# Performance work log

Measured on AMD Instinct MI355X. Metric: run time of the kernel, lower is better.

## Reference

```python
import jax, jax.numpy as jnp
import numpy as np

H = 128

def _gine_conv(x, ei, ea, w1, b1, w2, b2):
    # GINEConv (eps=0): out = MLP(x + sum_{j->i} relu(x_j + e_ji))
    src, dst = ei[0], ei[1]
    m = jax.nn.relu(x[src] + ea)                      # [E, H]
    agg = jax.ops.segment_sum(m, dst, num_segments=x.shape[0])
    h = x + agg
    return jax.nn.relu(h @ w1 + b1) @ w2 + b2

def _bn(x, gamma, beta, eps=1e-5):
    # BatchNorm1d over node dim, batch statistics (training mode)
    mu = jnp.mean(x, axis=0)
    var = jnp.mean((x - mu) ** 2, axis=0)
    return gamma * (x - mu) * jax.lax.rsqrt(var + eps) + beta

def _scatter_mean(vals, ids, mask, n):
    w = mask.astype(vals.dtype)
    s = jax.ops.segment_sum(vals * w[:, None], ids, num_segments=n)
    c = jax.ops.segment_sum(w, ids, num_segments=n)
    return s / jnp.maximum(c, 1.0)[:, None]


def setup_inputs() -> dict:
    key = jax.random.key(0)
    ks = jax.random.split(key, 20)
    Nf, Nt, S, K = 320000, 100000, 20000, 16
    Ei, Eg = 1280000, 800000
    sc = 1.0 / np.sqrt(H)
    inp = {}
    inp["h_flat"] = jax.random.normal(ks[0], (Nf, H), jnp.float32)
    inp["intra_ei"] = jax.random.randint(ks[1], (2, Ei), 0, Nf, jnp.int32)
    inp["ea_flat"] = jax.random.normal(ks[2], (Ei, H), jnp.float32)
    inp["valid"] = jnp.ones((Nf,), jnp.bool_)
    inp["node_ids"] = jax.random.randint(ks[3], (Nf,), 0, Nt, jnp.int32)
    inp["N_total"] = Nt
    inp["edge_index"] = jax.random.randint(ks[4], (2, Eg), 0, Nt, jnp.int32)
    inp["edge_attr"] = jax.random.normal(ks[5], (Eg, H), jnp.float32)
    inp["sub_batch"] = jax.random.randint(ks[6], (Nf,), 0, S, jnp.int32)
    inp["S"] = S
    inp["k"] = K
    inp["root_flat_idx"] = jax.random.randint(ks[7], (S,), 0, Nf, jnp.int32)
    inp["is_root"] = jnp.zeros((Nf,), jnp.bool_)
    # parameters
    inp["local_w1"] = jax.random.normal(ks[8], (H, H), jnp.float32) * sc
    inp["local_b1"] = jnp.zeros((H,), jnp.float32)
    inp["local_w2"] = jax.random.normal(ks[9], (H, H), jnp.float32) * sc
    inp["local_b2"] = jnp.zeros((H,), jnp.float32)
    inp["local_gamma"] = jnp.ones((H,), jnp.float32)
    inp["local_beta"] = jnp.zeros((H,), jnp.float32)
    inp["global_w1"] = jax.random.normal(ks[10], (H, H), jnp.float32) * sc
    inp["global_b1"] = jnp.zeros((H,), jnp.float32)
    inp["global_w2"] = jax.random.normal(ks[11], (H, H), jnp.float32) * sc
    inp["global_b2"] = jnp.zeros((H,), jnp.float32)
    inp["global_gamma"] = jnp.ones((H,), jnp.float32)
    inp["global_beta"] = jnp.zeros((H,), jnp.float32)
    inp["skip_w"] = jax.random.normal(ks[12], (H, H), jnp.float32) * sc
    inp["skip_b"] = jnp.zeros((H,), jnp.float32)
    inp["vv_w"] = jax.random.normal(ks[13], (H, H), jnp.float32) * sc
    inp["vv_b"] = jnp.zeros((H,), jnp.float32)
    inp["kk_w"] = jax.random.normal(ks[14], (H, H), jnp.float32) * sc
    inp["kk_b"] = jnp.zeros((H,), jnp.float32)
    return inp


def reference(h_flat, intra_ei, ea_flat, valid, node_ids, N_total, edge_index, edge_attr,
              sub_batch, S, k, root_flat_idx, is_root,
              local_w1, local_b1, local_w2, local_b2, local_gamma, local_beta,
              global_w1, global_b1, global_w2, global_b2, global_gamma, global_beta,
              skip_w, skip_b, vv_w, vv_b, kk_w, kk_b):
    valid_f = valid.astype(h_flat.dtype)[:, None]
    clamped_ids = jnp.maximum(node_ids, 0)
    valid_mask = node_ids >= 0

    h_skip = (h_flat @ skip_w + skip_b) * valid_f

    h1 = _gine_conv(h_flat, intra_ei, ea_flat, local_w1, local_b1, local_w2, local_b2)
    h1 = _bn(h1, local_gamma, local_beta) * valid_f

    x_sum = _scatter_mean(h_flat, clamped_ids, valid_mask, N_total)   # [N_total, H]
    h2 = _gine_conv(x_sum, edge_index, edge_attr, global_w1, global_b1, global_w2, global_b2)
    h2 = _bn(h2, global_gamma, global_beta)[clamped_ids] * valid_f

    root_ids = node_ids[root_flat_idx]
    root_valid = root_ids >= 0
    x_vv_canonical = _scatter_mean(h_flat[root_flat_idx], jnp.maximum(root_ids, 0), root_valid, N_total)
    x_vv = (x_vv_canonical[clamped_ids] @ vv_w + vv_b) * valid_f

    x_kk = (h_flat[root_flat_idx[sub_batch]] @ kk_w + kk_b) * valid_f

    out = jax.nn.relu(h_skip + h1 + h2 + x_vv + x_kk)
    # dropout p=0.0 -> identity
    return out * valid_f
```

## Files before the change

kernel.cpp:

```cpp
#include <hip/hip_runtime.h>

#define H    128
#define HQ   32
#define TM   64
#define NT   100000
#define XS   136


typedef __attribute__((ext_vector_type(8))) short short8;
typedef __attribute__((ext_vector_type(4))) float f32x4;

static __host__ int cdiv(long a, long b) { return (int)((a + b - 1) / b); }
static __host__ char* alignp(char* p) {
    return (char*)(((uintptr_t)p + 255) & ~(uintptr_t)255);
}

__device__ inline unsigned short f2bf(float f) {
    unsigned u = __float_as_uint(f);
    unsigned r = u + 0x7FFFu + ((u >> 16) & 1u);
    return (unsigned short)(r >> 16);
}
__device__ inline float bf2f(unsigned short u) {
    return __uint_as_float((unsigned)u << 16);
}

__global__ __launch_bounds__(256) void k_cvt(
    const float* __restrict__ in, unsigned short* __restrict__ out, long n8)
{
    long i = (long)blockIdx.x * 256 + threadIdx.x;
    if (i >= n8) return;
    float4 a = ((const float4*)in)[2 * i];
    float4 b = ((const float4*)in)[2 * i + 1];
    ushort4 lo; lo.x = f2bf(a.x); lo.y = f2bf(a.y); lo.z = f2bf(a.z); lo.w = f2bf(a.w);
    ushort4 hi; hi.x = f2bf(b.x); hi.y = f2bf(b.y); hi.z = f2bf(b.z); hi.w = f2bf(b.w);
    ((ushort4*)out)[2 * i]     = lo;
    ((ushort4*)out)[2 * i + 1] = hi;
}

struct WJobs { const float* src[7]; };

__global__ __launch_bounds__(256) void k_cvtw(WJobs wj, unsigned short* __restrict__ dstBase)
{
    int w = blockIdx.x >> 4, chunk = blockIdx.x & 15;
    int i = chunk * 256 + threadIdx.x;
    int k = i >> 5, n4 = (i & 31) * 4;
    float4 v = ((const float4*)wj.src[w])[i];
    unsigned short* dst = dstBase + (size_t)w * H * H;
    dst[(n4 + 0) * H + k] = f2bf(v.x);
    dst[(n4 + 1) * H + k] = f2bf(v.y);
    dst[(n4 + 2) * H + k] = f2bf(v.z);
    dst[(n4 + 3) * H + k] = f2bf(v.w);
}

struct CsrJobs {
    const int* ids[4];
    const int* rfi;
    int* cnt[4];
    int* rp[4];
    int* cur[4];
    int* eid[4];
    int  E[4];
    int  N[4];
    int  histBase[5];
    int  scanBase[5];
};

__device__ inline int csr_id(const CsrJobs& jb, int sg, int e)
{
    if (sg == 3) {
        int nid = jb.ids[2][jb.rfi[e]];
        return nid > 0 ? nid : 0;
    }
    return jb.ids[sg][e];
}

__global__ __launch_bounds__(256) void k_hist4(CsrJobs jb)
{
    int b = blockIdx.x, sg = 0;
    while (b >= jb.histBase[sg + 1]) ++sg;
    int e = (b - jb.histBase[sg]) * 256 + threadIdx.x;
    if (e < jb.E[sg]) atomicAdd(&jb.cnt[sg][csr_id(jb, sg, e)], 1);
}

__global__ __launch_bounds__(256) void k_scanA4(CsrJobs jb, int* __restrict__ parts)
{
    int b = blockIdx.x, sg = 0;
    while (b >= jb.scanBase[sg + 1]) ++sg;
    int lb = b - jb.scanBase[sg];
    const int* cnt = jb.cnt[sg];
    int* rowptr = jb.rp[sg];
    int N = jb.N[sg];
    int* partials = parts + sg * 256;

    __shared__ int lsum[256];
    int tid = threadIdx.x;
    int base = lb * 2048 + tid * 8;
    int v[8];
    int tsum = 0;
#pragma unroll
    for (int i = 0; i < 8; ++i) {
        int idx = base + i;
        int t = (idx < N) ? cnt[idx] : 0;
        v[i] = tsum;
        tsum += t;
    }
    lsum[tid] = tsum;
    __syncthreads();
    for (int off = 1; off < 256; off <<= 1) {
        int t = (tid >= off) ? lsum[tid - off] : 0;
        __syncthreads();
        lsum[tid] += t;
        __syncthreads();
    }
    int texcl = lsum[tid] - tsum;
#pragma unroll
    for (int i = 0; i < 8; ++i) {
        int idx = base + i;
        if (idx < N) rowptr[idx] = v[i] + texcl;
    }
    if (tid == 255) partials[lb] = lsum[255];
}

__global__ __launch_bounds__(256) void k_scanB4(CsrJobs jb, int* __restrict__ parts)
{
    int sg = blockIdx.x;
    int P = jb.scanBase[sg + 1] - jb.scanBase[sg];
    int* partials = parts + sg * 256;
    int* rowptr = jb.rp[sg];
    int N = jb.N[sg];

    __shared__ int lsum[256];
    int tid = threadIdx.x;
    int val = (tid < P) ? partials[tid] : 0;
    lsum[tid] = val;
    __syncthreads();
    for (int off = 1; off < 256; off <<= 1) {
        int t = (tid >= off) ? lsum[tid - off] : 0;
        __syncthreads();
        lsum[tid] += t;
        __syncthreads();
    }
    if (tid < P) partials[tid] = lsum[tid] - val;
    if (tid == 255) rowptr[N] = lsum[255];
}

__global__ __launch_bounds__(256) void k_scanC4(CsrJobs jb, const int* __restrict__ parts)
{
    int b = blockIdx.x, sg = 0;
    while (b >= jb.scanBase[sg + 1]) ++sg;
    int lb = b - jb.scanBase[sg];
    int off = parts[sg * 256 + lb];
    int N = jb.N[sg];
    int* rowptr = jb.rp[sg];
    int* cursor = jb.cur[sg];
    int base = lb * 2048;
    for (int i = threadIdx.x; i < 2048; i += 256) {
        int g = base + i;
        if (g < N) {
            int v = rowptr[g] + off;
            rowptr[g] = v;
            cursor[g] = v;
        }
    }
}

__global__ __launch_bounds__(256) void k_fillperm4(CsrJobs jb)
{
    int b = blockIdx.x, sg = 0;
    while (b >= jb.histBase[sg + 1]) ++sg;
    int e = (b - jb.histBase[sg]) * 256 + threadIdx.x;
    if (e < jb.E[sg]) {
        int pos = atomicAdd(&jb.cur[sg][csr_id(jb, sg, e)], 1);
        jb.eid[sg][pos] = e;
    }
}

__global__ __launch_bounds__(256) void k_csr_edge_agg(
    const unsigned short* __restrict__ X, const float* __restrict__ EA,
    const int* __restrict__ src, const int* __restrict__ eid,
    const int* __restrict__ rowptr, unsigned short* __restrict__ OUT, int N)
{
    int idx = blockIdx.x * 256 + threadIdx.x;
    int n = idx >> 5, l = idx & 31;
    if (n >= N) return;
    int beg = rowptr[n], end = rowptr[n + 1];
    float4 acc = {0.f, 0.f, 0.f, 0.f};
    for (int c0 = beg; c0 < end; c0 += 32) {
        int cnt = min(32, end - c0);
        int e_l = 0, s_l = 0;
        if (l < cnt) { e_l = eid[c0 + l]; s_l = src[e_l]; }
        for (int j = 0; j < cnt; ++j) {
            int e = __shfl(e_l, j, 32);
            int s = __shfl(s_l, j, 32);
            float4 a = ((const float4*)(EA + (size_t)e * H))[l];
            ushort4 h = ((const ushort4*)(X + (size_t)s * H))[l];
            acc.x += fmaxf(bf2f(h.x) + a.x, 0.f);
            acc.y += fmaxf(bf2f(h.y) + a.y, 0.f);
            acc.z += fmaxf(bf2f(h.z) + a.z, 0.f);
            acc.w += fmaxf(bf2f(h.w) + a.w, 0.f);
        }
    }
    ushort4 o;
    o.x = f2bf(acc.x); o.y = f2bf(acc.y); o.z = f2bf(acc.z); o.w = f2bf(acc.w);
    ((ushort4*)(OUT + (size_t)n * H))[l] = o;
}

__global__ __launch_bounds__(256) void k_csr_mean(
    const unsigned short* __restrict__ X, const int* __restrict__ eid,
    const int* __restrict__ rowptr, unsigned short* __restrict__ OUT, int N)
{
    int idx = blockIdx.x * 256 + threadIdx.x;
    int n = idx >> 5, l = idx & 31;
    if (n >= N) return;
    int beg = rowptr[n], end = rowptr[n + 1];
    float4 acc = {0.f, 0.f, 0.f, 0.f};
    for (int c0 = beg; c0 < end; c0 += 32) {
        int cnt = min(32, end - c0);
        int f_l = 0;
        if (l < cnt) f_l = eid[c0 + l];
        for (int j = 0; j < cnt; ++j) {
            int fi = __shfl(f_l, j, 32);
            ushort4 h = ((const ushort4*)(X + (size_t)fi * H))[l];
            acc.x += bf2f(h.x); acc.y += bf2f(h.y);
            acc.z += bf2f(h.z); acc.w += bf2f(h.w);
        }
    }
    float inv = 1.0f / fmaxf((float)(end - beg), 1.0f);
    ushort4 o;
    o.x = f2bf(acc.x * inv); o.y = f2bf(acc.y * inv);
    o.z = f2bf(acc.z * inv); o.w = f2bf(acc.w * inv);
    ((ushort4*)(OUT + (size_t)n * H))[l] = o;
}

__device__ inline void stage_x_copy(
    unsigned short* sX, const unsigned short* X1, const int* gidx,
    int r0, int M, int tid)
{
    int r = tid >> 2, q = tid & 3;
    int row = r0 + r;
    unsigned short* dst = &sX[r * XS + q * 32];
    if (row < M) {
        int sr = gidx ? gidx[row] : row;
        const ushort4* xp = (const ushort4*)(X1 + (size_t)sr * H + q * 32);
#pragma unroll
        for (int i = 0; i < 8; ++i) *(ushort4*)(dst + i * 4) = xp[i];
    } else {
#pragma unroll
        for (int i = 0; i < 8; ++i) *(ushort4*)(dst + i * 4) = ushort4{0, 0, 0, 0};
    }
}

__device__ inline void stage_x_sum(
    unsigned short* sX, const unsigned short* X1, const unsigned short* X2,
    int r0, int M, int tid)
{
    int r = tid >> 2, q = tid & 3;
    int row = r0 + r;
    unsigned short* dst = &sX[r * XS + q * 32];
    if (row < M) {
        const ushort4* xp = (const ushort4*)(X1 + (size_t)row * H + q * 32);
        const ushort4* yp = (const ushort4*)(X2 + (size_t)row * H + q * 32);
#pragma unroll
        for (int i = 0; i < 8; ++i) {
            ushort4 a = xp[i], b = yp[i];
            ushort4 o;
            o.x = f2bf(bf2f(a.x) + bf2f(b.x));
            o.y = f2bf(bf2f(a.y) + bf2f(b.y));
            o.z = f2bf(bf2f(a.z) + bf2f(b.z));
            o.w = f2bf(bf2f(a.w) + bf2f(b.w));
            *(ushort4*)(dst + i * 4) = o;
        }
    } else {
#pragma unroll
        for (int i = 0; i < 8; ++i) *(ushort4*)(dst + i * 4) = ushort4{0, 0, 0, 0};
    }
}

__device__ inline void stage_wt_pre(
    unsigned short* sWT, const unsigned short* WT, int tid)
{
    for (int i = tid; i < H * HQ; i += 256) {
        int n = i >> 5, kq = i & 31;
        *(ushort4*)&sWT[n * XS + kq * 4] = ((const ushort4*)WT)[i];
    }
}

__global__ __launch_bounds__(256) void k_gemm(
    const unsigned short* __restrict__ X1, const int* __restrict__ gidx,
    const unsigned short* __restrict__ WT, const float* __restrict__ B,
    unsigned short* __restrict__ OUT, int M)
{
    __shared__ unsigned short sX[TM * XS];
    __shared__ unsigned short sWT[H * XS];
    __shared__ float sB[H];
    int tid = threadIdx.x;
    int r0 = blockIdx.x * TM;

    stage_x_copy(sX, X1, gidx, r0, M, tid);
    stage_wt_pre(sWT, WT, tid);
    if (tid < 32) ((float4*)sB)[tid] = ((const float4*)B)[tid];
    __syncthreads();

    int wv = tid >> 6, l = tid & 63;
    int lr = l & 15, hi = l >> 4, lk = hi * 8;

    f32x4 acc[8];
#pragma unroll
    for (int ct = 0; ct < 8; ++ct) acc[ct] = {0.f, 0.f, 0.f, 0.f};
#pragma unroll
    for (int kk = 0; kk < 4; ++kk) {
        short8 a = *(const short8*)&sX[(wv * 16 + lr) * XS + kk * 32 + lk];
#pragma unroll
        for (int ct = 0; ct < 8; ++ct) {
            short8 b = *(const short8*)&sWT[(ct * 16 + lr) * XS + kk * 32 + lk];
            acc[ct] = __builtin_amdgcn_mfma_f32_16x16x32_bf16(a, b, acc[ct], 0, 0, 0);
        }
    }

    int orow0 = r0 + wv * 16 + hi * 4;
#pragma unroll
    for (int ct = 0; ct < 8; ++ct) {
        int col = ct * 16 + lr;
        float bias = sB[col];
#pragma unroll
        for (int j = 0; j < 4; ++j) {
            int row = orow0 + j;
            if (row >= M) continue;
            OUT[(size_t)row * H + col] = f2bf(acc[ct][j] + bias);
        }
    }
}

__global__ __launch_bounds__(256) void k_mean_gemm(
    const unsigned short* __restrict__ X, const int* __restrict__ eid,
    const int* __restrict__ rowmap, const int* __restrict__ rowptr,
    const unsigned short* __restrict__ WT, const float* __restrict__ B,
    unsigned short* __restrict__ OUT, int M)
{
    __shared__ unsigned short sX[TM * XS];
    __shared__ unsigned short sWT[H * XS];
    __shared__ float sB[H];
    int tid = threadIdx.x;
    int r0 = blockIdx.x * TM;

    {
        int r = tid >> 2, q = tid & 3;
        int row = r0 + r;
        float4 m[8];
#pragma unroll
        for (int i = 0; i < 8; ++i) m[i] = {0.f, 0.f, 0.f, 0.f};
        int cnt = 0;
        if (row < M) {
            int beg = rowptr[row], end = rowptr[row + 1];
            cnt = end - beg;
            for (int j = beg; j < end; ++j) {
                int fi = rowmap[eid[j]];
                const ushort4* hp = (const ushort4*)(X + (size_t)fi * H + q * 32);
#pragma unroll
                for (int i = 0; i < 8; ++i) {
                    ushort4 v = hp[i];
                    m[i].x += bf2f(v.x); m[i].y += bf2f(v.y);
                    m[i].z += bf2f(v.z); m[i].w += bf2f(v.w);
                }
            }
        }
        float inv = 1.0f / fmaxf((float)cnt, 1.0f);
        unsigned short* dst = &sX[r * XS + q * 32];
#pragma unroll
        for (int i = 0; i < 8; ++i) {
            ushort4 b;
            b.x = f2bf(m[i].x * inv); b.y = f2bf(m[i].y * inv);
            b.z = f2bf(m[i].z * inv); b.w = f2bf(m[i].w * inv);
            *(ushort4*)(dst + i * 4) = b;
        }
    }
    stage_wt_pre(sWT, WT, tid);
    if (tid < 32) ((float4*)sB)[tid] = ((const float4*)B)[tid];
    __syncthreads();

    int wv = tid >> 6, l = tid & 63;
    int lr = l & 15, hi = l >> 4, lk = hi * 8;

    f32x4 acc[8];
#pragma unroll
    for (int ct = 0; ct < 8; ++ct) acc[ct] = {0.f, 0.f, 0.f, 0.f};
#pragma unroll
    for (int kk = 0; kk < 4; ++kk) {
        short8 a = *(const short8*)&sX[(wv * 16 + lr) * XS + kk * 32 + lk];
#pragma unroll
        for (int ct = 0; ct < 8; ++ct) {
            short8 b = *(const short8*)&sWT[(ct * 16 + lr) * XS + kk * 32 + lk];
            acc[ct] = __builtin_amdgcn_mfma_f32_16x16x32_bf16(a, b, acc[ct], 0, 0, 0);
        }
    }

    int orow0 = r0 + wv * 16 + hi * 4;
#pragma unroll
    for (int ct = 0; ct < 8; ++ct) {
        int col = ct * 16 + lr;
        float bias = sB[col];
#pragma unroll
        for (int j = 0; j < 4; ++j) {
            int row = orow0 + j;
            if (row >= M) continue;
            OUT[(size_t)row * H + col] = f2bf(acc[ct][j] + bias);
        }
    }
}

__global__ __launch_bounds__(256) void k_mlp(
    const unsigned short* __restrict__ X1, const unsigned short* __restrict__ X2,
    const unsigned short* __restrict__ W1T, const float* __restrict__ B1,
    const unsigned short* __restrict__ W2T, const float* __restrict__ B2,
    unsigned short* __restrict__ OUT, int M,
    float* __restrict__ gs, float* __restrict__ gs2)
{
    __shared__ unsigned short sX[TM * XS];
    __shared__ unsigned short sWT[H * XS];
    __shared__ float sB1[H], sB2[H];
    __shared__ float sS[H], sS2[H];
    int tid = threadIdx.x;
    int r0 = blockIdx.x * TM;

    stage_x_sum(sX, X1, X2, r0, M, tid);
    stage_wt_pre(sWT, W1T, tid);
    if (tid < 32) ((float4*)sB1)[tid] = ((const float4*)B1)[tid];
    else if (tid < 64) ((float4*)sB2)[tid - 32] = ((const float4*)B2)[tid - 32];
    if (tid >= 64 && tid < 192) { sS[tid - 64] = 0.f; sS2[tid - 64] = 0.f; }
    __syncthreads();

    int wv = tid >> 6, l = tid & 63;
    int lr = l & 15, hi = l >> 4, lk = hi * 8;
    int rloc = wv * 16 + hi * 4;

    f32x4 acc[8];
#pragma unroll
    for (int ct = 0; ct < 8; ++ct) acc[ct] = {0.f, 0.f, 0.f, 0.f};
#pragma unroll
    for (int kk = 0; kk < 4; ++kk) {
        short8 a = *(const short8*)&sX[(wv * 16 + lr) * XS + kk * 32 + lk];
#pragma unroll
        for (int ct = 0; ct < 8; ++ct) {
            short8 b = *(const short8*)&sWT[(ct * 16 + lr) * XS + kk * 32 + lk];
            acc[ct] = __builtin_amdgcn_mfma_f32_16x16x32_bf16(a, b, acc[ct], 0, 0, 0);
        }
    }
    __syncthreads();

#pragma unroll
    for (int ct = 0; ct < 8; ++ct) {
        int c = ct * 16 + lr;
        float b1v = sB1[c];
#pragma unroll
        for (int j = 0; j < 4; ++j) {
            float v = fmaxf(acc[ct][j] + b1v, 0.f);
            int mybf = (int)f2bf(v);
            int other = __shfl_xor(mybf, 1);
            if (!(lr & 1)) {
                unsigned packed = (unsigned)(unsigned short)mybf
                                | ((unsigned)(unsigned short)other << 16);
                *(unsigned*)&sX[(rloc + j) * XS + c] = packed;
            }
        }
        acc[ct] = {0.f, 0.f, 0.f, 0.f};
    }
    stage_wt_pre(sWT, W2T, tid);
    __syncthreads();

#pragma unroll
    for (int kk = 0; kk < 4; ++kk) {
        short8 a = *(const short8*)&sX[(wv * 16 + lr) * XS + kk * 32 + lk];
#pragma unroll
        for (int ct = 0; ct < 8; ++ct) {
            short8 b = *(const short8*)&sWT[(ct * 16 + lr) * XS + kk * 32 + lk];
            acc[ct] = __builtin_amdgcn_mfma_f32_16x16x32_bf16(a, b, acc[ct], 0, 0, 0);
        }
    }

    int orow0 = r0 + rloc;
#pragma unroll
    for (int ct = 0; ct < 8; ++ct) {
        int col = ct * 16 + lr;
        float b2v = sB2[col];
        float ps = 0.f, ps2 = 0.f;
#pragma unroll
        for (int j = 0; j < 4; ++j) {
            int row = orow0 + j;
            if (row >= M) continue;
            float o = acc[ct][j] + b2v;
            OUT[(size_t)row * H + col] = f2bf(o);
            ps += o; ps2 += o * o;
        }
        atomicAdd(&sS[col], ps);
        atomicAdd(&sS2[col], ps2);
    }
    __syncthreads();
    if (tid < H) {
        unsafeAtomicAdd(&gs[tid], sS[tid]);
        unsafeAtomicAdd(&gs2[tid], sS2[tid]);
    }
}

__global__ __launch_bounds__(256) void k_final_gemm(
    const unsigned short* __restrict__ Hf,
    const unsigned short* __restrict__ SKWT, const float* __restrict__ SKB,
    const unsigned short* __restrict__ h1raw, const unsigned short* __restrict__ h2raw,
    const unsigned short* __restrict__ vvy, const unsigned short* __restrict__ kky,
    const int* __restrict__ node_ids, const int* __restrict__ sub_batch,
    const float* __restrict__ stats,
    const float* __restrict__ lg, const float* __restrict__ lbe,
    const float* __restrict__ gg, const float* __restrict__ gbe,
    float n1, float n2,
    float* __restrict__ OUT, int M)
{
    __shared__ unsigned short sX[TM * XS];
    __shared__ unsigned short sWT[H * XS];
    __shared__ float sP[5 * H];
    int tid = threadIdx.x;
    int r0 = blockIdx.x * TM;

    stage_x_copy(sX, Hf, nullptr, r0, M, tid);
    stage_wt_pre(sWT, SKWT, tid);
    if (tid < H) {
        float mu = stats[tid] / n1;
        float var = stats[H + tid] / n1 - mu * mu;
        float sc = lg[tid] * rsqrtf(var + 1e-5f);
        sP[tid] = sc; sP[H + tid] = lbe[tid] - mu * sc;
        mu = stats[2 * H + tid] / n2;
        var = stats[3 * H + tid] / n2 - mu * mu;
        sc = gg[tid] * rsqrtf(var + 1e-5f);
        sP[2 * H + tid] = sc; sP[3 * H + tid] = gbe[tid] - mu * sc;
    } else if (tid < H + 32) {
        ((float4*)(sP + 4 * H))[tid - H] = ((const float4*)SKB)[tid - H];
    }
    __syncthreads();

    int wv = tid >> 6, l = tid & 63;
    int lr = l & 15, hi = l >> 4, lk = hi * 8;

    f32x4 acc[8];
#pragma unroll
    for (int ct = 0; ct < 8; ++ct) acc[ct] = {0.f, 0.f, 0.f, 0.f};
#pragma unroll
    for (int kk = 0; kk < 4; ++kk) {
        short8 a = *(const short8*)&sX[(wv * 16 + lr) * XS + kk * 32 + lk];
#pragma unroll
        for (int ct = 0; ct < 8; ++ct) {
            short8 b = *(const short8*)&sWT[(ct * 16 + lr) * XS + kk * 32 + lk];
            acc[ct] = __builtin_amdgcn_mfma_f32_16x16x32_bf16(a, b, acc[ct], 0, 0, 0);
        }
    }
    __syncthreads();

    float* sF = (float*)sWT;
    int rloc0 = wv * 16 + hi * 4;
#pragma unroll
    for (int ct = 0; ct < 8; ++ct) {
        int col = ct * 16 + lr;
        float skbv = sP[4 * H + col];
#pragma unroll
        for (int j = 0; j < 4; ++j)
            sF[(rloc0 + j) * 130 + col] = acc[ct][j] + skbv;
    }
    __syncthreads();

    {
        int r = tid >> 2, q = tid & 3;
        int row = r0 + r;
        if (row < M) {
            int nid = node_ids[row];
            size_t cid = (size_t)(nid > 0 ? nid : 0);
            size_t sb  = (size_t)sub_batch[row];
            const ushort4* h1p = (const ushort4*)(h1raw + (size_t)row * H + q * 32);
            const ushort4* h2p = (const ushort4*)(h2raw + cid * H + q * 32);
            const ushort4* vvp = (const ushort4*)(vvy + cid * H + q * 32);
            const ushort4* kkp = (const ushort4*)(kky + sb * H + q * 32);
            float* op = OUT + (size_t)row * H + q * 32;
            const float* fr = &sF[r * 130 + q * 32];
#pragma unroll
            for (int i = 0; i < 8; ++i) {
                ushort4 a = h1p[i], b = h2p[i], c = vvp[i], d = kkp[i];
                int cb = q * 32 + i * 4;
                float4 o;
                o.x = fr[i * 4 + 0] + bf2f(a.x) * sP[cb + 0] + sP[H + cb + 0]
                    + bf2f(b.x) * sP[2 * H + cb + 0] + sP[3 * H + cb + 0]
                    + bf2f(c.x) + bf2f(d.x);
                o.y = fr[i * 4 + 1] + bf2f(a.y) * sP[cb + 1] + sP[H + cb + 1]
                    + bf2f(b.y) * sP[2 * H + cb + 1] + sP[3 * H + cb + 1]
                    + bf2f(c.y) + bf2f(d.y);
                o.z = fr[i * 4 + 2] + bf2f(a.z) * sP[cb + 2] + sP[H + cb + 2]
                    + bf2f(b.z) * sP[2 * H + cb + 2] + sP[3 * H + cb + 2]
                    + bf2f(c.z) + bf2f(d.z);
                o.w = fr[i * 4 + 3] + bf2f(a.w) * sP[cb + 3] + sP[H + cb + 3]
                    + bf2f(b.w) * sP[2 * H + cb + 3] + sP[3 * H + cb + 3]
                    + bf2f(c.w) + bf2f(d.w);
                o.x = fmaxf(o.x, 0.f); o.y = fmaxf(o.y, 0.f);
                o.z = fmaxf(o.z, 0.f); o.w = fmaxf(o.w, 0.f);
                ((float4*)op)[i] = o;
            }
        }
    }
}

extern "C" void kernel_launch(void* const* d_in, const int* in_sizes, int n_in,
                              void* d_out, int out_size, void* d_ws, size_t ws_size,
                              hipStream_t stream)
{
    const float* h_flat        = (const float*)d_in[0];
    const int*   intra_ei      = (const int*)d_in[1];
    const float* ea_flat       = (const float*)d_in[2];
    const int*   node_ids      = (const int*)d_in[4];
    const int*   edge_index    = (const int*)d_in[6];
    const float* edge_attr     = (const float*)d_in[7];
    const int*   sub_batch     = (const int*)d_in[8];
    const int*   root_flat_idx = (const int*)d_in[11];
    const float* lw1 = (const float*)d_in[13];
    const float* lb1 = (const float*)d_in[14];
    const float* lw2 = (const float*)d_in[15];
    const float* lb2 = (const float*)d_in[16];
    const float* lg  = (const float*)d_in[17];
    const float* lbe = (const float*)d_in[18];
    const float* gw1 = (const float*)d_in[19];
    const float* gb1 = (const float*)d_in[20];
    const float* gw2 = (const float*)d_in[21];
    const float* gb2 = (const float*)d_in[22];
    const float* gg  = (const float*)d_in[23];
    const float* gbe = (const float*)d_in[24];
    const float* skw = (const float*)d_in[25];
    const float* skb = (const float*)d_in[26];
    const float* vvw = (const float*)d_in[27];
    const float* vvb = (const float*)d_in[28];
    const float* kkw = (const float*)d_in[29];
    const float* kkb = (const float*)d_in[30];

    const int Nf = in_sizes[0] / H;
    const int Ei = in_sizes[2] / H;
    const int Eg = in_sizes[7] / H;
    const int S  = in_sizes[11];

    char* w = (char*)d_ws;
    unsigned short* hbf  = (unsigned short*)w; w += (size_t)Nf * H * 2;
    unsigned short* buf1 = (unsigned short*)w; w += (size_t)Nf * H * 2;
    unsigned short* xsum = (unsigned short*)w; w += (size_t)NT * H * 2;
    unsigned short* buf2 = (unsigned short*)w; w += (size_t)NT * H * 2;
    unsigned short* vvy  = (unsigned short*)w; w += (size_t)NT * H * 2;
    unsigned short* kbuf = (unsigned short*)w; w += (size_t)S * H * 2;
    unsigned short* wtb  = (unsigned short*)w; w += (size_t)7 * H * H * 2;
    w = alignp(w);
    int* cntAll = (int*)w; w += ((size_t)Nf + 3 * (size_t)NT) * 4;
    float* stats = (float*)w; w += 4 * H * 4;
    w = alignp(w);
    int* rpA  = (int*)w; w += ((size_t)Nf + 1) * 4;  w = alignp(w);
    int* rpB  = (int*)w; w += ((size_t)NT + 1) * 4;  w = alignp(w);
    int* rpC  = (int*)w; w += ((size_t)NT + 1) * 4;  w = alignp(w);
    int* rpD  = (int*)w; w += ((size_t)NT + 1) * 4;  w = alignp(w);
    int* curA = (int*)w; w += (size_t)Nf * 4;
    int* curB = (int*)w; w += (size_t)NT * 4;
    int* curC = (int*)w; w += (size_t)NT * 4;
    int* curD = (int*)w; w += (size_t)NT * 4;
    int* eidA = (int*)w; w += (size_t)Ei * 4;
    int* eidB = (int*)w; w += (size_t)Eg * 4;
    int* eidC = (int*)w; w += (size_t)Nf * 4;
    int* eidD = (int*)w; w += (size_t)S * 4;
    int* parts = (int*)w; w += 4 * 256 * 4;
    int* cntA = cntAll;
    int* cntB = cntA + Nf;
    int* cntC = cntB + NT;
    int* cntD = cntC + NT;

    hipMemsetAsync(cntAll, 0, ((size_t)Nf + 3 * (size_t)NT) * 4 + 4 * H * 4, stream);

    k_cvt<<<cdiv((long)Nf * H / 8, 256), 256, 0, stream>>>(
        h_flat, hbf, (long)Nf * H / 8);
    WJobs wj;
    wj.src[0] = lw1; wj.src[1] = lw2; wj.src[2] = gw1; wj.src[3] = gw2;
    wj.src[4] = skw; wj.src[5] = vvw; wj.src[6] = kkw;
    k_cvtw<<<7 * 16, 256, 0, stream>>>(wj, wtb);

    CsrJobs jb;
    jb.ids[0] = intra_ei + Ei;  jb.ids[1] = edge_index + Eg;
    jb.ids[2] = node_ids;       jb.ids[3] = nullptr;
    jb.rfi = root_flat_idx;
    jb.cnt[0] = cntA; jb.cnt[1] = cntB; jb.cnt[2] = cntC; jb.cnt[3] = cntD;
    jb.rp[0]  = rpA;  jb.rp[1]  = rpB;  jb.rp[2]  = rpC;  jb.rp[3]  = rpD;
    jb.cur[0] = curA; jb.cur[1] = curB; jb.cur[2] = curC; jb.cur[3] = curD;
    jb.eid[0] = eidA; jb.eid[1] = eidB; jb.eid[2] = eidC; jb.eid[3] = eidD;
    jb.E[0] = Ei; jb.E[1] = Eg; jb.E[2] = Nf; jb.E[3] = S;
    jb.N[0] = Nf; jb.N[1] = NT; jb.N[2] = NT; jb.N[3] = NT;
    jb.histBase[0] = 0;
    for (int i = 0; i < 4; ++i) jb.histBase[i + 1] = jb.histBase[i] + cdiv(jb.E[i], 256);
    jb.scanBase[0] = 0;
    for (int i = 0; i < 4; ++i) jb.scanBase[i + 1] = jb.scanBase[i] + cdiv(jb.N[i], 2048);

    k_hist4<<<jb.histBase[4], 256, 0, stream>>>(jb);
    k_scanA4<<<jb.scanBase[4], 256, 0, stream>>>(jb, parts);
    k_scanB4<<<4, 256, 0, stream>>>(jb, parts);
    k_scanC4<<<jb.scanBase[4], 256, 0, stream>>>(jb, parts);
    k_fillperm4<<<jb.histBase[4], 256, 0, stream>>>(jb);

    k_csr_mean<<<cdiv((long)NT * 32, 256), 256, 0, stream>>>(
        hbf, eidC, rpC, xsum, NT);
    k_csr_edge_agg<<<cdiv((long)Nf * 32, 256), 256, 0, stream>>>(
        hbf, ea_flat, intra_ei, eidA, rpA, buf1, Nf);
    k_csr_edge_agg<<<cdiv((long)NT * 32, 256), 256, 0, stream>>>(
        xsum, edge_attr, edge_index, eidB, rpB, buf2, NT);

    k_mlp<<<cdiv(Nf, TM), 256, 0, stream>>>(hbf, buf1, wtb + 0 * H * H, lb1,
                                            wtb + 1 * H * H, lb2,
                                            buf1, Nf, stats, stats + H);
    k_mlp<<<cdiv(NT, TM), 256, 0, stream>>>(xsum, buf2, wtb + 2 * H * H, gb1,
                                            wtb + 3 * H * H, gb2,
                                            buf2, NT, stats + 2 * H, stats + 3 * H);

    k_mean_gemm<<<cdiv(NT, TM), 256, 0, stream>>>(
        hbf, eidD, root_flat_idx, rpD, wtb + 5 * H * H, vvb, vvy, NT);
    k_gemm<<<cdiv(S, TM), 256, 0, stream>>>(hbf, root_flat_idx,
                                            wtb + 6 * H * H, kkb, kbuf, S);

    k_final_gemm<<<cdiv(Nf, TM), 256, 0, stream>>>(
        hbf, wtb + 4 * H * H, skb, buf1, buf2, vvy, kbuf, node_ids, sub_batch,
        stats, lg, lbe, gg, gbe, (float)Nf, (float)NT, (float*)d_out, Nf);
}
```

Baseline: 1.295 ms.

## Fuse GINE edge aggregation into MLP staging and merge conversion kernels

Removes the separate CSR edge-aggregation kernels and does the gather/relu/sum inside the MLP kernel's shared-memory staging, so the aggregated bf16 buffer is never written to or read back from global memory. Each thread now handles a quarter row and walks all incoming edges serially. This replaces the old layout where 32 lanes split a row and shared index loads via shuffles, so per-thread latency and load imbalance go up. It also merges the activation and weight bf16 conversion kernels into one launch. Rounding changes slightly: x + agg is now summed in fp32 before a single bf16 rounding.

```diff
diff --git a/kernel.cpp b/kernel.cpp
--- a/kernel.cpp
+++ b/kernel.cpp
@@ -24,32 +24,33 @@
     return __uint_as_float((unsigned)u << 16);
 }
 
-__global__ __launch_bounds__(256) void k_cvt(
-    const float* __restrict__ in, unsigned short* __restrict__ out, long n8)
-{
-    long i = (long)blockIdx.x * 256 + threadIdx.x;
-    if (i >= n8) return;
-    float4 a = ((const float4*)in)[2 * i];
-    float4 b = ((const float4*)in)[2 * i + 1];
-    ushort4 lo; lo.x = f2bf(a.x); lo.y = f2bf(a.y); lo.z = f2bf(a.z); lo.w = f2bf(a.w);
-    ushort4 hi; hi.x = f2bf(b.x); hi.y = f2bf(b.y); hi.z = f2bf(b.z); hi.w = f2bf(b.w);
-    ((ushort4*)out)[2 * i]     = lo;
-    ((ushort4*)out)[2 * i + 1] = hi;
-}
-
 struct WJobs { const float* src[7]; };
 
-__global__ __launch_bounds__(256) void k_cvtw(WJobs wj, unsigned short* __restrict__ dstBase)
-{
-    int w = blockIdx.x >> 4, chunk = blockIdx.x & 15;
-    int i = chunk * 256 + threadIdx.x;
-    int k = i >> 5, n4 = (i & 31) * 4;
-    float4 v = ((const float4*)wj.src[w])[i];
-    unsigned short* dst = dstBase + (size_t)w * H * H;
-    dst[(n4 + 0) * H + k] = f2bf(v.x);
-    dst[(n4 + 1) * H + k] = f2bf(v.y);
-    dst[(n4 + 2) * H + k] = f2bf(v.z);
-    dst[(n4 + 3) * H + k] = f2bf(v.w);
+__global__ __launch_bounds__(256) void k_cvt_all(
+    const float* __restrict__ in, unsigned short* __restrict__ out, long n8,
+    WJobs wj, unsigned short* __restrict__ dstBase, int nCvt)
+{
+    if ((int)blockIdx.x < nCvt) {
+        long i = (long)blockIdx.x * 256 + threadIdx.x;
+        if (i >= n8) return;
+        float4 a = ((const float4*)in)[2 * i];
+        float4 b = ((const float4*)in)[2 * i + 1];
+        ushort4 lo; lo.x = f2bf(a.x); lo.y = f2bf(a.y); lo.z = f2bf(a.z); lo.w = f2bf(a.w);
+        ushort4 hi; hi.x = f2bf(b.x); hi.y = f2bf(b.y); hi.z = f2bf(b.z); hi.w = f2bf(b.w);
+        ((ushort4*)out)[2 * i]     = lo;
+        ((ushort4*)out)[2 * i + 1] = hi;
+    } else {
+        int b = blockIdx.x - nCvt;
+        int w = b >> 4, chunk = b & 15;
+        int i = chunk * 256 + threadIdx.x;
+        int k = i >> 5, n4 = (i & 31) * 4;
+        float4 v = ((const float4*)wj.src[w])[i];
+        unsigned short* dst = dstBase + (size_t)w * H * H;
+        dst[(n4 + 0) * H + k] = f2bf(v.x);
+        dst[(n4 + 1) * H + k] = f2bf(v.y);
+        dst[(n4 + 2) * H + k] = f2bf(v.z);
+        dst[(n4 + 3) * H + k] = f2bf(v.w);
+    }
 }
 
 struct CsrJobs {
@@ -175,36 +176,6 @@
     }
 }
 
-__global__ __launch_bounds__(256) void k_csr_edge_agg(
-    const unsigned short* __restrict__ X, const float* __restrict__ EA,
-    const int* __restrict__ src, const int* __restrict__ eid,
-    const int* __restrict__ rowptr, unsigned short* __restrict__ OUT, int N)
-{
-    int idx = blockIdx.x * 256 + threadIdx.x;
-    int n = idx >> 5, l = idx & 31;
-    if (n >= N) return;
-    int beg = rowptr[n], end = rowptr[n + 1];
-    float4 acc = {0.f, 0.f, 0.f, 0.f};
-    for (int c0 = beg; c0 < end; c0 += 32) {
-        int cnt = min(32, end - c0);
-        int e_l = 0, s_l = 0;
-        if (l < cnt) { e_l = eid[c0 + l]; s_l = src[e_l]; }
-        for (int j = 0; j < cnt; ++j) {
-            int e = __shfl(e_l, j, 32);
-            int s = __shfl(s_l, j, 32);
-            float4 a = ((const float4*)(EA + (size_t)e * H))[l];
-            ushort4 h = ((const ushort4*)(X + (size_t)s * H))[l];
-            acc.x += fmaxf(bf2f(h.x) + a.x, 0.f);
-            acc.y += fmaxf(bf2f(h.y) + a.y, 0.f);
-            acc.z += fmaxf(bf2f(h.z) + a.z, 0.f);
-            acc.w += fmaxf(bf2f(h.w) + a.w, 0.f);
-        }
-    }
-    ushort4 o;
-    o.x = f2bf(acc.x); o.y = f2bf(acc.y); o.z = f2bf(acc.z); o.w = f2bf(acc.w);
-    ((ushort4*)(OUT + (size_t)n * H))[l] = o;
-}
-
 __global__ __launch_bounds__(256) void k_csr_mean(
     const unsigned short* __restrict__ X, const int* __restrict__ eid,
     const int* __restrict__ rowptr, unsigned short* __restrict__ OUT, int N)
@@ -250,25 +221,45 @@
     }
 }
 
-__device__ inline void stage_x_sum(
-    unsigned short* sX, const unsigned short* X1, const unsigned short* X2,
+__device__ inline void stage_x_agg(
+    unsigned short* sX, const unsigned short* X1, const float* EA,
+    const int* src, const int* eid, const int* rowptr,
     int r0, int M, int tid)
 {
     int r = tid >> 2, q = tid & 3;
     int row = r0 + r;
     unsigned short* dst = &sX[r * XS + q * 32];
     if (row < M) {
+        float4 m[8];
         const ushort4* xp = (const ushort4*)(X1 + (size_t)row * H + q * 32);
-        const ushort4* yp = (const ushort4*)(X2 + (size_t)row * H + q * 32);
 #pragma unroll
         for (int i = 0; i < 8; ++i) {
-            ushort4 a = xp[i], b = yp[i];
-            ushort4 o;
-            o.x = f2bf(bf2f(a.x) + bf2f(b.x));
-            o.y = f2bf(bf2f(a.y) + bf2f(b.y));
-            o.z = f2bf(bf2f(a.z) + bf2f(b.z));
-            o.w = f2bf(bf2f(a.w) + bf2f(b.w));
-            *(ushort4*)(dst + i * 4) = o;
+            ushort4 v = xp[i];
+            m[i].x = bf2f(v.x); m[i].y = bf2f(v.y);
+            m[i].z = bf2f(v.z); m[i].w = bf2f(v.w);
+        }
+        int beg = rowptr[row], end = rowptr[row + 1];
+        for (int j = beg; j < end; ++j) {
+            int e = eid[j];
+            int s = src[e];
+            const float4* ep = (const float4*)(EA + (size_t)e * H) + q * 8;
+            const ushort4* hp = (const ushort4*)(X1 + (size_t)s * H + q * 32);
+#pragma unroll
+            for (int i = 0; i < 8; ++i) {
+                float4 a = ep[i];
+                ushort4 h = hp[i];
+                m[i].x += fmaxf(bf2f(h.x) + a.x, 0.f);
+                m[i].y += fmaxf(bf2f(h.y) + a.y, 0.f);
+                m[i].z += fmaxf(bf2f(h.z) + a.z, 0.f);
+                m[i].w += fmaxf(bf2f(h.w) + a.w, 0.f);
+            }
+        }
+#pragma unroll
+        for (int i = 0; i < 8; ++i) {
+            ushort4 b;
+            b.x = f2bf(m[i].x); b.y = f2bf(m[i].y);
+            b.z = f2bf(m[i].z); b.w = f2bf(m[i].w);
+            *(ushort4*)(dst + i * 4) = b;
         }
     } else {
 #pragma unroll
@@ -408,8 +399,10 @@
     }
 }
 
-__global__ __launch_bounds__(256) void k_mlp(
-    const unsigned short* __restrict__ X1, const unsigned short* __restrict__ X2,
+__global__ __launch_bounds__(256) void k_mlp_agg(
+    const unsigned short* __restrict__ X1,
+    const float* __restrict__ EA, const int* __restrict__ src,
+    const int* __restrict__ eid, const int* __restrict__ rowptr,
     const unsigned short* __restrict__ W1T, const float* __restrict__ B1,
     const unsigned short* __restrict__ W2T, const float* __restrict__ B2,
     unsigned short* __restrict__ OUT, int M,
@@ -422,7 +415,7 @@
     int tid = threadIdx.x;
     int r0 = blockIdx.x * TM;
 
-    stage_x_sum(sX, X1, X2, r0, M, tid);
+    stage_x_agg(sX, X1, EA, src, eid, rowptr, r0, M, tid);
     stage_wt_pre(sWT, W1T, tid);
     if (tid < 32) ((float4*)sB1)[tid] = ((const float4*)B1)[tid];
     else if (tid < 64) ((float4*)sB2)[tid - 32] = ((const float4*)B2)[tid - 32];
@@ -670,12 +663,12 @@
 
     hipMemsetAsync(cntAll, 0, ((size_t)Nf + 3 * (size_t)NT) * 4 + 4 * H * 4, stream);
 
-    k_cvt<<<cdiv((long)Nf * H / 8, 256), 256, 0, stream>>>(
-        h_flat, hbf, (long)Nf * H / 8);
     WJobs wj;
     wj.src[0] = lw1; wj.src[1] = lw2; wj.src[2] = gw1; wj.src[3] = gw2;
     wj.src[4] = skw; wj.src[5] = vvw; wj.src[6] = kkw;
-    k_cvtw<<<7 * 16, 256, 0, stream>>>(wj, wtb);
+    int nCvt = cdiv((long)Nf * H / 8, 256);
+    k_cvt_all<<<nCvt + 7 * 16, 256, 0, stream>>>(
+        h_flat, hbf, (long)Nf * H / 8, wj, wtb, nCvt);
 
     CsrJobs jb;
     jb.ids[0] = intra_ei + Ei;  jb.ids[1] = edge_index + Eg;
@@ -700,17 +693,15 @@
 
     k_csr_mean<<<cdiv((long)NT * 32, 256), 256, 0, stream>>>(
         hbf, eidC, rpC, xsum, NT);
-    k_csr_edge_agg<<<cdiv((long)Nf * 32, 256), 256, 0, stream>>>(
-        hbf, ea_flat, intra_ei, eidA, rpA, buf1, Nf);
-    k_csr_edge_agg<<<cdiv((long)NT * 32, 256), 256, 0, stream>>>(
-        xsum, edge_attr, edge_index, eidB, rpB, buf2, NT);
-
-    k_mlp<<<cdiv(Nf, TM), 256, 0, stream>>>(hbf, buf1, wtb + 0 * H * H, lb1,
-                                            wtb + 1 * H * H, lb2,
-                                            buf1, Nf, stats, stats + H);
-    k_mlp<<<cdiv(NT, TM), 256, 0, stream>>>(xsum, buf2, wtb + 2 * H * H, gb1,
-                                            wtb + 3 * H * H, gb2,
-                                            buf2, NT, stats + 2 * H, stats + 3 * H);
+
+    k_mlp_agg<<<cdiv(Nf, TM), 256, 0, stream>>>(
+        hbf, ea_flat, intra_ei, eidA, rpA,
+        wtb + 0 * H * H, lb1, wtb + 1 * H * H, lb2,
+        buf1, Nf, stats, stats + H);
+    k_mlp_agg<<<cdiv(NT, TM), 256, 0, stream>>>(
+        xsum, edge_attr, edge_index, eidB, rpB,
+        wtb + 2 * H * H, gb1, wtb + 3 * H * H, gb2,
+        buf2, NT, stats + 2 * H, stats + 3 * H);
 
     k_mean_gemm<<<cdiv(NT, TM), 256, 0, stream>>>(
         hbf, eidD, root_flat_idx, rpD, wtb + 5 * H * H, vvb, vvy, NT);
```

After: 1.264 ms. -2.4%, faster.
